# Kernel optimization log

Hardware: AMD Instinct MI355X
Metric: run time of the kernel (lower is better)

The kernel has to match this reference:

```python
import jax, jax.numpy as jnp
import numpy as np

B, S, D, H = 16, 784, 768, 12
DH = D // H  # 64


def rotate_half(x):
    # (x1, x2, x3, x4) -> (-x2, x1, -x4, x3), interleaved
    x_even = x[..., ::2]
    x_odd = x[..., 1::2]
    return jnp.stack((-x_odd, x_even), axis=-1).reshape(x.shape)


def setup_inputs() -> dict:
    key = jax.random.key(0)
    ks = jax.random.split(key, 12)
    s = 0.02
    return {
        "hidden_states": jax.random.normal(ks[0], (B, S, D), jnp.float32),
        "rotary_pos_emb": jax.random.uniform(ks[1], (B, S, DH), jnp.float32) * 6.28,
        "wq": jax.random.normal(ks[2], (D, D), jnp.float32) * s,
        "bq": jax.random.normal(ks[3], (D,), jnp.float32) * s,
        "wk": jax.random.normal(ks[4], (D, D), jnp.float32) * s,
        "bk": jax.random.normal(ks[5], (D,), jnp.float32) * s,
        "wv": jax.random.normal(ks[6], (D, D), jnp.float32) * s,
        "bv": jax.random.normal(ks[7], (D,), jnp.float32) * s,
        "wo": jax.random.normal(ks[8], (D, D), jnp.float32) * s,
        "bo": jax.random.normal(ks[9], (D,), jnp.float32) * s,
    }


def reference(hidden_states, rotary_pos_emb, wq, bq, wk, bk, wv, bv, wo, bo):
    scale = DH ** -0.5
    # Linear: x @ W^T + b; reshape to [B, H, S, DH]
    def proj(w, b):
        y = jnp.einsum("bsd,ed->bse", hidden_states, w) + b
        return y.reshape(B, S, H, DH).transpose(0, 2, 1, 3)

    q = proj(wq, bq)
    k = proj(wk, bk)
    v = proj(wv, bv)

    # RoPE: freqs [B, S, DH] -> [B, 1, S, DH] broadcast over heads
    cos = jnp.cos(rotary_pos_emb)[:, None, :, :]
    sin = jnp.sin(rotary_pos_emb)[:, None, :, :]
    q = q * cos + rotate_half(q) * sin
    k = k * cos + rotate_half(k) * sin

    attn = jnp.einsum("bhqd,bhkd->bhqk", q, k) * scale
    attn = jax.nn.softmax(attn, axis=-1)
    out = jnp.einsum("bhqk,bhkd->bhqd", attn, v)
    out = out.transpose(0, 2, 1, 3).reshape(B, S, D)
    out = jnp.einsum("bsd,ed->bse", out, wo) + bo
    return out
```

## Files before the change

kernel.cpp:

```cpp
#include <hip/hip_runtime.h>
#include <cstdint>
#include <cstddef>

constexpr int kB  = 16;
constexpr int kS  = 784;
constexpr int kD  = 768;
constexpr int kH  = 12;
constexpr int kM  = kB * kS;
constexpr int kSP = 832;

typedef __attribute__((ext_vector_type(8))) short bf16x8;
typedef __attribute__((ext_vector_type(4))) float floatx4;

__device__ __forceinline__ unsigned short f2bf(float x) {
    union { float f; unsigned int u; } v; v.f = x;
    unsigned int r = v.u + 0x7fffu + ((v.u >> 16) & 1u);
    return (unsigned short)(r >> 16);
}
__device__ __forceinline__ float bf2f(unsigned short h) {
    union { unsigned int u; float f; } v; v.u = ((unsigned int)h) << 16;
    return v.f;
}

__device__ __forceinline__ void gload_lds16(const void* g, void* l) {
    __builtin_amdgcn_global_load_lds(
        (const __attribute__((address_space(1))) void*)g,
        (__attribute__((address_space(3))) void*)l,
        16, 0, 0);
}

constexpr int kHsF4   = (kM * kD) / 4;
constexpr int kWF4    = (kD * kD) / 4;
constexpr int kPreTot = kHsF4 + 4 * kWF4 + (kM * 64) / 4;

__global__ __launch_bounds__(256)
void convert_pre(const float* __restrict__ hs, const float* __restrict__ rot,
                 const float* __restrict__ wq, const float* __restrict__ wk,
                 const float* __restrict__ wv, const float* __restrict__ wo,
                 const float* __restrict__ bq, const float* __restrict__ bk,
                 const float* __restrict__ bv,
                 unsigned short* __restrict__ hsB, unsigned short* __restrict__ wB,
                 unsigned int* __restrict__ csT, float* __restrict__ biasC)
{
    const int i = blockIdx.x * 256 + threadIdx.x;
    if (i < kHsF4) {
        float4 v = ((const float4*)hs)[i];
        ushort4 o = { f2bf(v.x), f2bf(v.y), f2bf(v.z), f2bf(v.w) };
        ((ushort4*)hsB)[i] = o;
    } else if (i < kHsF4 + 4 * kWF4) {
        const int j = i - kHsF4;
        const int w = j / kWF4, jj = j - w * kWF4;
        const float* src = (w == 0) ? wq : (w == 1) ? wk : (w == 2) ? wv : wo;
        float4 v = ((const float4*)src)[jj];
        ushort4 o = { f2bf(v.x), f2bf(v.y), f2bf(v.z), f2bf(v.w) };
        ((ushort4*)(wB + (size_t)w * (kD * kD)))[jj] = o;
    } else if (i < kPreTot) {
        const int j = i - kHsF4 - 4 * kWF4;
        float4 v = ((const float4*)rot)[j];
        float a[4] = { v.x, v.y, v.z, v.w };
        #pragma unroll
        for (int e = 0; e < 4; ++e) {
            float s, c;
            __sincosf(a[e], &s, &c);
            csT[j * 4 + e] = (unsigned)f2bf(c) | ((unsigned)f2bf(s) << 16);
        }
    } else {
        const int j = i - kPreTot;
        if (j < 3 * kD)
            biasC[j] = (j < kD) ? bq[j] : (j < 2 * kD) ? bk[j - kD] : bv[j - 2 * kD];
    }
}

enum { MODE_QKV = 0, MODE_OUT = 1 };

template<int MODE>
__global__ __launch_bounds__(256, 2)
void gemm_k(const unsigned short* __restrict__ A, const unsigned short* __restrict__ W,
            const float* __restrict__ bias, const unsigned int* __restrict__ csT,
            unsigned short* __restrict__ Qp, unsigned short* __restrict__ Kp,
            unsigned short* __restrict__ Vtp, float* __restrict__ Op)
{
    constexpr int BN  = (MODE == MODE_QKV) ? 256 : 128;
    constexpr int NTL = (MODE == MODE_QKV) ? 9 : 6;
    constexpr int NTC = BN / 32;
    constexpr int WJ  = BN / 64;

    __shared__ unsigned short As[2][4096];
    __shared__ unsigned short Ws[2][BN * 32];

    const int lin   = blockIdx.x;
    const int group = lin / (8 * NTL);
    const int rem   = lin - group * (8 * NTL);
    const int base_m = group * 8;
    int m_tile, n_tile;
    if (base_m + 8 <= 98) { m_tile = base_m + (rem & 7); n_tile = rem >> 3; }
    else                  { m_tile = base_m + (rem & 1); n_tile = rem >> 1; }
    const int m0 = m_tile * 128;
    const int n0 = n_tile * BN;

    const int tid  = threadIdx.x;
    const int wave = tid >> 6;
    const int lane = tid & 63;
    const int quad = lane >> 4;
    const int l16  = lane & 15;
    const int wm = wave >> 1, wn = wave & 1;

    floatx4 acc[4][NTC];
    #pragma unroll
    for (int mt = 0; mt < 4; ++mt)
        #pragma unroll
        for (int nt = 0; nt < NTC; ++nt)
            acc[mt][nt] = {0.f, 0.f, 0.f, 0.f};

    const int sidx0 = wave * 128 + lane;
    const int srow0 = sidx0 >> 2, sseg0 = (sidx0 & 3) ^ ((srow0 >> 1) & 3);
    const int sidx1 = sidx0 + 64;
    const int srow1 = sidx1 >> 2, sseg1 = (sidx1 & 3) ^ ((srow1 >> 1) & 3);
    int wrow[WJ], wseg[WJ];
    #pragma unroll
    for (int j = 0; j < WJ; ++j) {
        const int cid = wave * BN + j * 64 + lane;
        wrow[j] = cid >> 2;
        wseg[j] = (cid & 3) ^ ((wrow[j] >> 1) & 3);
    }

    gload_lds16(A + (size_t)(m0 + srow0) * kD + sseg0 * 8, &As[0][wave * 1024]);
    gload_lds16(A + (size_t)(m0 + srow1) * kD + sseg1 * 8, &As[0][wave * 1024 + 512]);
    #pragma unroll
    for (int j = 0; j < WJ; ++j)
        gload_lds16(W + (size_t)(n0 + wrow[j]) * kD + wseg[j] * 8,
                    &Ws[0][(wave * BN + j * 64) * 8]);

    for (int ks = 0; ks < 24; ++ks) {
        __syncthreads();
        if (ks < 23) {
            const int nb = (ks + 1) & 1;
            const int k0 = (ks + 1) * 32;
            gload_lds16(A + (size_t)(m0 + srow0) * kD + k0 + sseg0 * 8, &As[nb][wave * 1024]);
            gload_lds16(A + (size_t)(m0 + srow1) * kD + k0 + sseg1 * 8, &As[nb][wave * 1024 + 512]);
            #pragma unroll
            for (int j = 0; j < WJ; ++j)
                gload_lds16(W + (size_t)(n0 + wrow[j]) * kD + k0 + wseg[j] * 8,
                            &Ws[nb][(wave * BN + j * 64) * 8]);
        }
        const unsigned short* as_ = As[ks & 1];
        const unsigned short* ws_ = Ws[ks & 1];

        bf16x8 af[4], bw[NTC];
        #pragma unroll
        for (int mt = 0; mt < 4; ++mt) {
            const int row = wm * 64 + mt * 16 + l16;
            const int slot = quad ^ ((row >> 1) & 3);
            af[mt] = *(const bf16x8*)&as_[row * 32 + slot * 8];
        }
        #pragma unroll
        for (int nt = 0; nt < NTC; ++nt) {
            const int row = wn * (BN / 2) + nt * 16 + l16;
            const int slot = quad ^ ((row >> 1) & 3);
            bw[nt] = *(const bf16x8*)&ws_[row * 32 + slot * 8];
        }
        #pragma unroll
        for (int mt = 0; mt < 4; ++mt)
            #pragma unroll
            for (int nt = 0; nt < NTC; ++nt)
                acc[mt][nt] = __builtin_amdgcn_mfma_f32_16x16x32_bf16(
                    af[mt], bw[nt], acc[mt][nt], 0, 0, 0);
    }

    if constexpr (MODE == MODE_OUT) {
        #pragma unroll
        for (int nt = 0; nt < NTC; ++nt) {
            const int n = n0 + wn * (BN / 2) + nt * 16 + l16;
            const float bv = bias[n];
            #pragma unroll
            for (int mt = 0; mt < 4; ++mt)
                #pragma unroll
                for (int r = 0; r < 4; ++r) {
                    const int m = m0 + wm * 64 + mt * 16 + quad * 4 + r;
                    Op[(size_t)m * kD + n] = acc[mt][nt][r] + bv;
                }
        }
    } else {
        const int proj = n_tile / 3;
        if (proj < 2) {
            unsigned short* dst = proj ? Kp : Qp;
            const float scale = proj ? 1.0f : 0.125f;
            #pragma unroll
            for (int nt = 0; nt < NTC; ++nt) {
                const int n = n0 + wn * (BN / 2) + nt * 16 + l16;
                const float bv = bias[n];
                const int col = n - proj * kD;
                const int dh = col & 63;
                const int odd = l16 & 1;
                #pragma unroll
                for (int mt = 0; mt < 4; ++mt)
                    #pragma unroll
                    for (int r = 0; r < 4; ++r) {
                        const int m = m0 + wm * 64 + mt * 16 + quad * 4 + r;
                        const float val = acc[mt][nt][r] + bv;
                        const float px = __shfl_xor(val, 1);
                        const unsigned u = csT[(size_t)m * 64 + dh];
                        const float c = bf2f((unsigned short)(u & 0xffffu));
                        const float s = bf2f((unsigned short)(u >> 16));
                        const float out = odd ? (val * c + px * s) : (val * c - px * s);
                        dst[(size_t)m * kD + col] = f2bf(out * scale);
                    }
            }
        } else {
            #pragma unroll
            for (int nt = 0; nt < NTC; ++nt) {
                const int n = n0 + wn * (BN / 2) + nt * 16 + l16;
                const float bv = bias[n];
                const int col = n - 2 * kD;
                const int h = col >> 6, dh = col & 63;
                #pragma unroll
                for (int mt = 0; mt < 4; ++mt) {
                    const int m_r0 = m0 + wm * 64 + mt * 16 + quad * 4;
                    const int b = m_r0 / kS;
                    const int s = m_r0 - b * kS;
                    ushort4 pk;
                    pk.x = f2bf(acc[mt][nt][0] + bv);
                    pk.y = f2bf(acc[mt][nt][1] + bv);
                    pk.z = f2bf(acc[mt][nt][2] + bv);
                    pk.w = f2bf(acc[mt][nt][3] + bv);
                    *(ushort4*)(Vtp + (size_t)((b * kH + h) * 64 + dh) * kSP + s) = pk;
                }
            }
        }
    }
}

__global__ __launch_bounds__(256)
void flash_attn(const unsigned short* __restrict__ Qg,
                const unsigned short* __restrict__ Kg,
                const unsigned short* __restrict__ Vtg,
                unsigned short* __restrict__ Og)
{
    __shared__ unsigned short KV[2][8192];
    __shared__ unsigned short Ps[4][32 * 68];

    const int lin   = blockIdx.x;
    const int group = lin / 56;
    const int rem   = lin - group * 56;
    const int bh = group * 8 + (rem & 7);
    const int qt = rem >> 3;
    const int b = bh / kH, h = bh - b * kH;
    const int tid = threadIdx.x, wave = tid >> 6, lane = tid & 63;
    const int quad = lane >> 4, l16 = lane & 15;
    const int q0 = qt * 128;
    const size_t rowBase = (size_t)(b * kS) * kD + h * 64;

    #pragma unroll
    for (int j = 0; j < 4; ++j) {
        const int idx = (wave * 4 + j) * 64 + lane;
        const int row = idx >> 3, slot = idx & 7, seg = slot ^ (row & 7);
        gload_lds16(Qg + rowBase + (size_t)(q0 + row) * kD + seg * 8,
                    &KV[0][(wave * 4 + j) * 512]);
    }
    __syncthreads();
    bf16x8 aq[2][2];
    #pragma unroll
    for (int mt = 0; mt < 2; ++mt)
        #pragma unroll
        for (int ch = 0; ch < 2; ++ch) {
            const int row = wave * 32 + mt * 16 + l16;
            const int slot = (ch * 4 + quad) ^ (row & 7);
            aq[mt][ch] = *(const bf16x8*)&KV[0][row * 64 + slot * 8];
        }
    __syncthreads();

    const int cidx0 = wave * 128 + lane;
    const int crow0 = cidx0 >> 3, cseg0 = (cidx0 & 7) ^ (crow0 & 7);
    const int cidx1 = cidx0 + 64;
    const int crow1 = cidx1 >> 3, cseg1 = (cidx1 & 7) ^ (crow1 & 7);

    {
        gload_lds16(Kg + rowBase + (size_t)(crow0)*kD + cseg0 * 8, &KV[0][wave * 1024]);
        gload_lds16(Vtg + (size_t)(bh * 64 + crow0) * kSP + cseg0 * 8, &KV[0][4096 + wave * 1024]);
        gload_lds16(Kg + rowBase + (size_t)(crow1)*kD + cseg1 * 8, &KV[0][wave * 1024 + 512]);
        gload_lds16(Vtg + (size_t)(bh * 64 + crow1) * kSP + cseg1 * 8, &KV[0][4096 + wave * 1024 + 512]);
    }

    floatx4 oacc[2][4];
    #pragma unroll
    for (int mt = 0; mt < 2; ++mt)
        #pragma unroll
        for (int nt = 0; nt < 4; ++nt)
            oacc[mt][nt] = {0.f, 0.f, 0.f, 0.f};
    float lrow[2][4];
    #pragma unroll
    for (int mt = 0; mt < 2; ++mt)
        #pragma unroll
        for (int r = 0; r < 4; ++r) lrow[mt][r] = 0.f;

    for (int kt = 0; kt < 13; ++kt) {
        __syncthreads();
        if (kt < 12) {
            const int nb = (kt + 1) & 1;
            const int kr = (kt + 1) * 64;
            gload_lds16(Kg + rowBase + (size_t)(kr + crow0) * kD + cseg0 * 8,
                        &KV[nb][wave * 1024]);
            gload_lds16(Vtg + (size_t)(bh * 64 + crow0) * kSP + kr + cseg0 * 8,
                        &KV[nb][4096 + wave * 1024]);
            gload_lds16(Kg + rowBase + (size_t)(kr + crow1) * kD + cseg1 * 8,
                        &KV[nb][wave * 1024 + 512]);
            gload_lds16(Vtg + (size_t)(bh * 64 + crow1) * kSP + kr + cseg1 * 8,
                        &KV[nb][4096 + wave * 1024 + 512]);
        }
        const unsigned short* Ks = &KV[kt & 1][0];
        const unsigned short* Vs = &KV[kt & 1][4096];

        bf16x8 bk[4][2];
        #pragma unroll
        for (int nt = 0; nt < 4; ++nt)
            #pragma unroll
            for (int ch = 0; ch < 2; ++ch) {
                const int row = nt * 16 + l16;
                const int slot = (ch * 4 + quad) ^ (row & 7);
                bk[nt][ch] = *(const bf16x8*)&Ks[row * 64 + slot * 8];
            }

        floatx4 sc[2][4];
        #pragma unroll
        for (int mt = 0; mt < 2; ++mt)
            #pragma unroll
            for (int nt = 0; nt < 4; ++nt) {
                sc[mt][nt] = {0.f, 0.f, 0.f, 0.f};
                sc[mt][nt] = __builtin_amdgcn_mfma_f32_16x16x32_bf16(
                    aq[mt][0], bk[nt][0], sc[mt][nt], 0, 0, 0);
                sc[mt][nt] = __builtin_amdgcn_mfma_f32_16x16x32_bf16(
                    aq[mt][1], bk[nt][1], sc[mt][nt], 0, 0, 0);
            }

        if (kt == 12) {
            #pragma unroll
            for (int mt = 0; mt < 2; ++mt)
                #pragma unroll
                for (int nt = 1; nt < 4; ++nt)
                    #pragma unroll
                    for (int r = 0; r < 4; ++r) sc[mt][nt][r] = -1e30f;
        }

        #pragma unroll
        for (int mt = 0; mt < 2; ++mt)
            #pragma unroll
            for (int nt = 0; nt < 4; ++nt)
                #pragma unroll
                for (int r = 0; r < 4; ++r) {
                    const float p = __expf(sc[mt][nt][r]);
                    union { float f; unsigned u; } pu; pu.f = p;
                    union { unsigned u; float f; } pt; pt.u = pu.u & 0xFFFF0000u;
                    lrow[mt][r] += pt.f;
                    Ps[wave][(mt * 16 + quad * 4 + r) * 68 + nt * 16 + l16] =
                        (unsigned short)(pu.u >> 16);
                }

        bf16x8 ap[2][2];
        #pragma unroll
        for (int mt = 0; mt < 2; ++mt)
            #pragma unroll
            for (int ks = 0; ks < 2; ++ks)
                ap[mt][ks] = *(const bf16x8*)&Ps[wave][(mt * 16 + l16) * 68 + ks * 32 + quad * 8];

        #pragma unroll
        for (int ks = 0; ks < 2; ++ks)
            #pragma unroll
            for (int nt = 0; nt < 4; ++nt) {
                const int row = nt * 16 + l16;
                const int slot = (ks * 4 + quad) ^ (row & 7);
                const bf16x8 bv = *(const bf16x8*)&Vs[row * 64 + slot * 8];
                #pragma unroll
                for (int mt = 0; mt < 2; ++mt)
                    oacc[mt][nt] = __builtin_amdgcn_mfma_f32_16x16x32_bf16(
                        ap[mt][ks], bv, oacc[mt][nt], 0, 0, 0);
            }
    }

    #pragma unroll
    for (int mt = 0; mt < 2; ++mt)
        #pragma unroll
        for (int r = 0; r < 4; ++r) {
            float l = lrow[mt][r];
            #pragma unroll
            for (int off = 1; off < 16; off <<= 1) l += __shfl_xor(l, off);
            lrow[mt][r] = 1.0f / l;
        }

    #pragma unroll
    for (int mt = 0; mt < 2; ++mt)
        #pragma unroll
        for (int r = 0; r < 4; ++r) {
            const int srow = q0 + wave * 32 + mt * 16 + quad * 4 + r;
            if (srow < kS) {
                const float inv = lrow[mt][r];
                #pragma unroll
                for (int nt = 0; nt < 4; ++nt)
                    Og[rowBase + (size_t)srow * kD + nt * 16 + l16] =
                        f2bf(oacc[mt][nt][r] * inv);
            }
        }
}

extern "C" void kernel_launch(void* const* d_in, const int* in_sizes, int n_in,
                              void* d_out, int out_size, void* d_ws, size_t ws_size,
                              hipStream_t stream)
{
    (void)in_sizes; (void)n_in; (void)out_size; (void)ws_size;
    const float* hs  = (const float*)d_in[0];
    const float* rot = (const float*)d_in[1];
    const float* wq  = (const float*)d_in[2];
    const float* bq  = (const float*)d_in[3];
    const float* wk  = (const float*)d_in[4];
    const float* bk  = (const float*)d_in[5];
    const float* wv  = (const float*)d_in[6];
    const float* bv  = (const float*)d_in[7];
    const float* wo  = (const float*)d_in[8];
    const float* bo  = (const float*)d_in[9];

    char* ws = (char*)d_ws;
    unsigned short* hsB  = (unsigned short*)ws;
    unsigned short* wB   = (unsigned short*)(ws + 19267584);
    unsigned int*   csT  = (unsigned int*)(ws + 23986176);
    float*          biasC= (float*)(ws + 27197440);
    unsigned short* Q    = (unsigned short*)(ws + 27206656);
    unsigned short* K    = (unsigned short*)(ws + 46474240);
    unsigned short* Vt   = (unsigned short*)(ws + 65741824);
    unsigned short* O    = hsB;

    const dim3 blk(256);

    convert_pre<<<dim3(12505), blk, 0, stream>>>(hs, rot, wq, wk, wv, wo, bq, bk, bv,
                                                 hsB, wB, csT, biasC);
    gemm_k<MODE_QKV><<<dim3(882), blk, 0, stream>>>(
        hsB, wB, biasC, csT, Q, K, Vt, nullptr);
    flash_attn<<<dim3(7 * 192), blk, 0, stream>>>(Q, K, Vt, O);
    gemm_k<MODE_OUT><<<dim3(588), blk, 0, stream>>>(
        O, wB + 3 * kD * kD, bo, nullptr, nullptr, nullptr, nullptr, (float*)d_out);
}
```

Baseline: 276.2 us.

## Replace direct-to-LDS double buffering with register-staged two-deep prefetch in GEMM

The GEMM main loop stops using global_load_lds into double-buffered LDS. It now loads tiles into registers two k-steps ahead and writes them to a single LDS buffer each iteration, with barriers before and after compute. This halves LDS use and raises prefetch depth to hide global latency, but adds register pressure, explicit LDS stores and a second barrier per iteration.

```diff
diff --git a/kernel.cpp b/kernel.cpp
--- a/kernel.cpp
+++ b/kernel.cpp
@@ -20,6 +20,10 @@
 __device__ __forceinline__ float bf2f(unsigned short h) {
     union { unsigned int u; float f; } v; v.u = ((unsigned int)h) << 16;
     return v.f;
+}
+
+__device__ __forceinline__ void barrier_lds() {
+    asm volatile("s_waitcnt lgkmcnt(0)\n\ts_barrier" ::: "memory");
 }
 
 __device__ __forceinline__ void gload_lds16(const void* g, void* l) {
@@ -83,10 +87,10 @@
     constexpr int BN  = (MODE == MODE_QKV) ? 256 : 128;
     constexpr int NTL = (MODE == MODE_QKV) ? 9 : 6;
     constexpr int NTC = BN / 32;
-    constexpr int WJ  = BN / 64;
-
-    __shared__ unsigned short As[2][4096];
-    __shared__ unsigned short Ws[2][BN * 32];
+    constexpr int CW  = BN / 64;
+
+    __shared__ unsigned short As[128 * 32];
+    __shared__ unsigned short Ws[BN * 32];
 
     const int lin   = blockIdx.x;
     const int group = lin / (8 * NTL);
@@ -112,52 +116,64 @@
         for (int nt = 0; nt < NTC; ++nt)
             acc[mt][nt] = {0.f, 0.f, 0.f, 0.f};
 
-    const int sidx0 = wave * 128 + lane;
-    const int srow0 = sidx0 >> 2, sseg0 = (sidx0 & 3) ^ ((srow0 >> 1) & 3);
-    const int sidx1 = sidx0 + 64;
-    const int srow1 = sidx1 >> 2, sseg1 = (sidx1 & 3) ^ ((srow1 >> 1) & 3);
-    int wrow[WJ], wseg[WJ];
-    #pragma unroll
-    for (int j = 0; j < WJ; ++j) {
-        const int cid = wave * BN + j * 64 + lane;
-        wrow[j] = cid >> 2;
-        wseg[j] = (cid & 3) ^ ((wrow[j] >> 1) & 3);
-    }
-
-    gload_lds16(A + (size_t)(m0 + srow0) * kD + sseg0 * 8, &As[0][wave * 1024]);
-    gload_lds16(A + (size_t)(m0 + srow1) * kD + sseg1 * 8, &As[0][wave * 1024 + 512]);
-    #pragma unroll
-    for (int j = 0; j < WJ; ++j)
-        gload_lds16(W + (size_t)(n0 + wrow[j]) * kD + wseg[j] * 8,
-                    &Ws[0][(wave * BN + j * 64) * 8]);
+    int arow[2], aseg[2];
+    #pragma unroll
+    for (int j = 0; j < 2; ++j) {
+        const int cid = j * 256 + tid;
+        arow[j] = cid >> 2;
+        aseg[j] = (cid & 3) ^ ((arow[j] >> 1) & 3);
+    }
+    int wrow_[CW], wseg_[CW];
+    #pragma unroll
+    for (int j = 0; j < CW; ++j) {
+        const int cid = j * 256 + tid;
+        wrow_[j] = cid >> 2;
+        wseg_[j] = (cid & 3) ^ ((wrow_[j] >> 1) & 3);
+    }
+
+    uint4 rA[2][2], rW[2][CW];
+    #pragma unroll
+    for (int s = 0; s < 2; ++s) {
+        const int k0 = s * 32;
+        #pragma unroll
+        for (int j = 0; j < 2; ++j)
+            rA[s][j] = *(const uint4*)(A + (size_t)(m0 + arow[j]) * kD + k0 + aseg[j] * 8);
+        #pragma unroll
+        for (int j = 0; j < CW; ++j)
+            rW[s][j] = *(const uint4*)(W + (size_t)(n0 + wrow_[j]) * kD + k0 + wseg_[j] * 8);
+    }
 
     for (int ks = 0; ks < 24; ++ks) {
-        __syncthreads();
-        if (ks < 23) {
-            const int nb = (ks + 1) & 1;
-            const int k0 = (ks + 1) * 32;
-            gload_lds16(A + (size_t)(m0 + srow0) * kD + k0 + sseg0 * 8, &As[nb][wave * 1024]);
-            gload_lds16(A + (size_t)(m0 + srow1) * kD + k0 + sseg1 * 8, &As[nb][wave * 1024 + 512]);
-            #pragma unroll
-            for (int j = 0; j < WJ; ++j)
-                gload_lds16(W + (size_t)(n0 + wrow[j]) * kD + k0 + wseg[j] * 8,
-                            &Ws[nb][(wave * BN + j * 64) * 8]);
-        }
-        const unsigned short* as_ = As[ks & 1];
-        const unsigned short* ws_ = Ws[ks & 1];
+        const int s = ks & 1;
+        #pragma unroll
+        for (int j = 0; j < 2; ++j)
+            *(uint4*)&As[(j * 256 + tid) * 8] = rA[s][j];
+        #pragma unroll
+        for (int j = 0; j < CW; ++j)
+            *(uint4*)&Ws[(j * 256 + tid) * 8] = rW[s][j];
+        if (ks < 22) {
+            const int k0 = (ks + 2) * 32;
+            #pragma unroll
+            for (int j = 0; j < 2; ++j)
+                rA[s][j] = *(const uint4*)(A + (size_t)(m0 + arow[j]) * kD + k0 + aseg[j] * 8);
+            #pragma unroll
+            for (int j = 0; j < CW; ++j)
+                rW[s][j] = *(const uint4*)(W + (size_t)(n0 + wrow_[j]) * kD + k0 + wseg_[j] * 8);
+        }
+        barrier_lds();
 
         bf16x8 af[4], bw[NTC];
         #pragma unroll
         for (int mt = 0; mt < 4; ++mt) {
             const int row = wm * 64 + mt * 16 + l16;
             const int slot = quad ^ ((row >> 1) & 3);
-            af[mt] = *(const bf16x8*)&as_[row * 32 + slot * 8];
+            af[mt] = *(const bf16x8*)&As[row * 32 + slot * 8];
         }
         #pragma unroll
         for (int nt = 0; nt < NTC; ++nt) {
             const int row = wn * (BN / 2) + nt * 16 + l16;
             const int slot = quad ^ ((row >> 1) & 3);
-            bw[nt] = *(const bf16x8*)&ws_[row * 32 + slot * 8];
+            bw[nt] = *(const bf16x8*)&Ws[row * 32 + slot * 8];
         }
         #pragma unroll
         for (int mt = 0; mt < 4; ++mt)
@@ -165,6 +181,8 @@
             for (int nt = 0; nt < NTC; ++nt)
                 acc[mt][nt] = __builtin_amdgcn_mfma_f32_16x16x32_bf16(
                     af[mt], bw[nt], acc[mt][nt], 0, 0, 0);
+
+        barrier_lds();
     }
 
     if constexpr (MODE == MODE_OUT) {
```

After: 484.3 us. +75.4%, slower.
